# Kernel optimization log

Hardware: AMD Instinct MI355X
Metric: run time of the kernel (lower is better)

## Reference

```python
import jax, jax.numpy as jnp
import numpy as np
import math

N = 131072   # number of points
C = 32       # embed_dim
K = 19       # num_class
ZD = 16      # z_dim
BN_EPS = 1e-4
SIG_THR = 0.8


def setup_inputs():
    key = jax.random.key(0)
    ks = jax.random.split(key, 16)
    f32 = jnp.float32
    rn = lambda k, s, sc=1.0: jax.random.normal(k, s, dtype=f32) * sc
    return {
        'feat': rn(ks[0], (N, C)),
        'scene_flow': rn(ks[1], (N, 3)),
        'coarse_pred': rn(ks[2], (N, K)),
        'z': rn(ks[3], (ZD,)),
        'select_w1': rn(ks[4], (C, C), 0.2),
        'bn_gamma': jnp.ones((C,), f32),
        'bn_beta': jnp.zeros((C,), f32),
        'bn_mean': jnp.zeros((C,), f32),
        'bn_var': jnp.ones((C,), f32),
        'select_w2': rn(ks[5], (C, 1), 0.2),
        'select_b2': jnp.zeros((1,), f32),
        'wq': rn(ks[6], (C, C), 0.2), 'bq': jnp.zeros((C,), f32),
        'wk': rn(ks[7], (C, C), 0.2), 'bk': jnp.zeros((C,), f32),
        'wv': rn(ks[8], (C, C), 0.2), 'bv': jnp.zeros((C,), f32),
        'wo': rn(ks[9], (C, C), 0.2), 'bo': jnp.zeros((C,), f32),
        'wt': rn(ks[10], (2 * C, C), 0.2), 'bt': jnp.zeros((C,), f32),
        'w_out': rn(ks[11], (C, K), 0.2), 'b_out': jnp.zeros((K,), f32),
        'w_gen': rn(ks[12], (ZD + K + 3, C), 0.2), 'b_gen': jnp.zeros((C,), f32),
    }


def _forward(feat, scene_flow, coarse_pred, z, select_w1, bn_gamma, bn_beta,
             bn_mean, bn_var, select_w2, select_b2, wq, bq, wk, bk, wv, bv,
             wo, bo, wt, bt, w_out, b_out, w_gen, b_gen):
    cp = jax.nn.softmax(coarse_pred, axis=-1)                      # (N, K)
    temp_mask = jnp.any(scene_flow != 0, axis=-1)                  # (N,)
    # select_mlp: Linear(no bias) -> BatchNorm(eval, eps=1e-4) -> ReLU -> Linear -> Sigmoid
    h = (feat @ select_w1 - bn_mean) / jnp.sqrt(bn_var + BN_EPS) * bn_gamma + bn_beta
    h = jnp.maximum(h, 0.0)
    score = jax.nn.sigmoid(h @ select_w2 + select_b2)[:, 0]        # (N,)
    valid = (score < SIG_THR) & temp_mask                          # (N,)
    # cvae stand-in: linear over concat(z, onehot(class), scene_flow) -> (N, K, C)
    wz, wc, ws = w_gen[:ZD], w_gen[ZD:ZD + K], w_gen[ZD + K:]
    gen = (z @ wz + b_gen)[None, None, :] + wc[None, :, :] + (scene_flow @ ws)[:, None, :]
    gen = gen * cp[:, :, None]                                     # scale by softmax prob
    # tiny cross-attention: 1 query per point over K=19 class prototypes
    q = feat @ wq + bq                                             # (N, C)
    k_ = jnp.einsum('nkc,cd->nkd', gen, wk) + bk                   # (N, K, C)
    v_ = jnp.einsum('nkc,cd->nkd', gen, wv) + bv                   # (N, K, C)
    attn = jax.nn.softmax(jnp.einsum('nd,nkd->nk', q, k_) / math.sqrt(C), axis=-1)
    aug = jnp.einsum('nk,nkd->nd', attn, v_) @ wo + bo             # (N, C)
    # scatter-back: invalid points get zeros (equivalent to torch boolean scatter)
    new_feat = jnp.where(valid[:, None], aug, 0.0)
    refine = jnp.concatenate([feat, new_feat], axis=-1) @ wt + bt  # (N, C)
    return refine @ w_out + b_out                                  # (N, K)


def reference(feat, scene_flow, coarse_pred, z, select_w1, bn_gamma, bn_beta,
              bn_mean, bn_var, select_w2, select_b2, wq, bq, wk, bk, wv, bv,
              wo, bo, wt, bt, w_out, b_out, w_gen, b_gen):
    return _forward(feat, scene_flow, coarse_pred, z, select_w1, bn_gamma,
                    bn_beta, bn_mean, bn_var, select_w2, select_b2, wq, bq,
                    wk, bk, wv, bv, wo, bo, wt, bt, w_out, b_out, w_gen, b_gen)
```

## Files before the change

### kernel.cpp

```cpp
#include <hip/hip_runtime.h>

#define NPTS 131072

typedef __attribute__((ext_vector_type(8))) short short8;
typedef __attribute__((ext_vector_type(4))) float f32x4;

constexpr int OFF_SW1 = 0;
constexpr int OFF_BNS = 1024;
constexpr int OFF_BNH = 1056;
constexpr int OFF_SW2 = 1088;
constexpr int OFF_B2  = 1120;
constexpr int OFF_QGB = 1121;
constexpr int OFF_QMB = 1140;
constexpr int OFF_BB  = 1143;
constexpr int OFF_CV  = 1162;
constexpr int OFF_MVB = 1181;
constexpr int EGVB    = 1240;
constexpr int FRAGH   = 1620;
constexpr int FRAGL   = 2900;
constexpr int XA1 = 3412, XA2 = 4020, XG = 4628, XMK = 5236, XMV = 5332;
constexpr int XGK = 5428, XGV = 6036, XB = 6644, XQG = 7252, XQM = 7860;

#define CONST_AS __attribute__((address_space(4)))
__device__ __forceinline__ const CONST_AS float* to_const(const float* p) {
    return (const CONST_AS float*)p;
}
__device__ __forceinline__ unsigned b16r(float x) {
    unsigned u = __float_as_uint(x);
    return (u + 0x7fffu + ((u >> 16) & 1u)) >> 16;
}
__device__ __forceinline__ float fromb(unsigned h) {
    return __uint_as_float(h << 16);
}

__global__ __launch_bounds__(256) void pre_a(
    const float* __restrict__ z,
    const float* __restrict__ sw1,
    const float* __restrict__ bn_gamma, const float* __restrict__ bn_beta,
    const float* __restrict__ bn_mean,  const float* __restrict__ bn_var,
    const float* __restrict__ sw2,      const float* __restrict__ sb2,
    const float* __restrict__ wk, const float* __restrict__ wv,
    const float* __restrict__ wt, const float* __restrict__ bt,
    const float* __restrict__ wout, const float* __restrict__ bout,
    const float* __restrict__ wgen, const float* __restrict__ bgen,
    float* __restrict__ W)
{
    int i = blockIdx.x * 256 + threadIdx.x;
    if (i < 1024) {
        W[OFF_SW1 + i] = sw1[(i & 31) * 32 + (i >> 5)];
    } else if (i < 1632) {
        int t = i - 1024, e = t / 19, j = t % 19;
        float a1 = 0.f, a2 = 0.f;
        for (int d = 0; d < 32; ++d) {
            float w_ = wout[d*19 + j];
            a1 += wt[e*32 + d] * w_;
            a2 += wt[(32 + e)*32 + d] * w_;
        }
        W[XA1 + t] = a1; W[XA2 + t] = a2;
    } else if (i < 2240) {
        int t = i - 1632, k = t >> 5, e = t & 31;
        float g = bgen[e];
        for (int d = 0; d < 16; ++d) g += z[d] * wgen[d*32 + e];
        W[XG + t] = g + wgen[(16 + k)*32 + e];
    } else if (i < 2336) {
        int t = i - 2240, m = t >> 5, c = t & 31;
        float a = 0.f, b = 0.f;
        for (int e = 0; e < 32; ++e) {
            float wsr = wgen[(35 + m)*32 + e];
            a += wsr * wk[e*32 + c];
            b += wsr * wv[e*32 + c];
        }
        W[XMK + t] = a; W[XMV + t] = b;
    } else if (i < 2368) {
        int t = i - 2336;
        float scale = bn_gamma[t] / sqrtf(bn_var[t] + 1e-4f);
        W[OFF_BNS + t] = scale;
        W[OFF_BNH + t] = bn_beta[t] - bn_mean[t] * scale;
        W[OFF_SW2 + t] = sw2[t];
    } else if (i < 2387) {
        int t = i - 2368;
        float a = bout[t];
        for (int d = 0; d < 32; ++d) a += bt[d] * wout[d*19 + t];
        W[OFF_BB + t] = a;
    } else if (i == 2387) {
        W[OFF_B2] = sb2[0];
    }
}

__global__ __launch_bounds__(256) void pre_b(
    const float* __restrict__ wq, const float* __restrict__ bq,
    const float* __restrict__ wk, const float* __restrict__ wv,
    const float* __restrict__ wo,
    float* __restrict__ W)
{
    int i = blockIdx.x * 256 + threadIdx.x;
    if (i < 608) {
        int k = i >> 5, c = i & 31;
        float a = 0.f, b = 0.f;
        for (int e = 0; e < 32; ++e) {
            float g = W[XG + k*32 + e];
            a += g * wk[e*32 + c];
            b += g * wv[e*32 + c];
        }
        W[XGK + i] = a; W[XGV + i] = b;
    } else if (i < 1216) {
        int t = i - 608, c = t / 19, j = t % 19;
        float a = 0.f;
        for (int d = 0; d < 32; ++d) a += wo[c*32 + d] * W[XA2 + d*19 + j];
        W[XB + t] = a;
    } else if (i < 1312) {
        int t = i - 1216, e = t / 3, m = t % 3;
        float a = 0.f;
        for (int c = 0; c < 32; ++c) a += wq[e*32 + c] * W[XMK + m*32 + c];
        W[XQM + t] = a;
    } else if (i < 1315) {
        int m = i - 1312;
        float a = 0.f;
        for (int c = 0; c < 32; ++c) a += bq[c] * W[XMK + m*32 + c];
        W[OFF_QMB + m] = a;
    }
}

__global__ __launch_bounds__(256) void pre_c(
    const float* __restrict__ wq, const float* __restrict__ bq,
    const float* __restrict__ bv, const float* __restrict__ bo,
    float* __restrict__ W)
{
    int i = blockIdx.x * 256 + threadIdx.x;
    if (i < 608) {
        int e = i / 19, k = i % 19;
        float a = 0.f;
        for (int c = 0; c < 32; ++c) a += wq[e*32 + c] * W[XGK + k*32 + c];
        W[XQG + i] = a;
    } else if (i < 627) {
        int k = i - 608;
        float a = 0.f;
        for (int c = 0; c < 32; ++c) a += bq[c] * W[XGK + k*32 + c];
        W[OFF_QGB + k] = a;
    } else if (i < 988) {
        int t = i - 627, k = t / 19, j = t % 19;
        float a = 0.f;
        for (int c = 0; c < 32; ++c) a += W[XGV + k*32 + c] * W[XB + c*19 + j];
        W[EGVB + k*20 + j] = a;
    } else if (i < 1007) {
        int k = i - 988;
        W[EGVB + k*20 + 19] = 0.f;
    } else if (i < 1064) {
        int t = i - 1007, m = t / 19, j = t % 19;
        float a = 0.f;
        for (int c = 0; c < 32; ++c) a += W[XMV + m*32 + c] * W[XB + c*19 + j];
        W[OFF_MVB + t] = a;
    } else if (i < 1083) {
        int j = i - 1064;
        float a = 0.f;
        for (int c = 0; c < 32; ++c) a += bv[c] * W[XB + c*19 + j];
        for (int d = 0; d < 32; ++d) a += bo[d] * W[XA2 + d*19 + j];
        W[OFF_CV + j] = a;
    }
}

__global__ __launch_bounds__(256) void pre_d(
    const float* __restrict__ sw1, float* __restrict__ W)
{
    int i = blockIdx.x * 256 + threadIdx.x;
    unsigned short* FH = (unsigned short*)(W + FRAGH);
    unsigned short* FL = (unsigned short*)(W + FRAGL);
    if (i < 2560) {
        int T = i >> 9, l = (i >> 3) & 63, j = i & 7;
        int e = ((l >> 4) << 3) + j, col = 16*T + (l & 15);
        float v;
        if      (col < 32) v = sw1[e*32 + col];
        else if (col < 51) v = W[XQG + e*19 + (col - 32)];
        else if (col < 70) v = W[XA1 + e*19 + (col - 51)];
        else if (col < 73) v = W[XQM + e*3  + (col - 70)];
        else               v = 0.f;
        FH[(T*64 + l)*8 + j] = (unsigned short)b16r(v);
    } else if (i < 3584) {
        int i2 = i - 2560;
        int T = i2 >> 9, l = (i2 >> 3) & 63, j = i2 & 7;
        int e = ((l >> 4) << 3) + j, col = 16*T + (l & 15);
        float v = sw1[e*32 + col];
        float vh = fromb(b16r(v));
        FL[(T*64 + l)*8 + j] = (unsigned short)b16r(v - vh);
    }
}

__global__ __launch_bounds__(256, 2) void main_k(
    const float* __restrict__ feat,
    const float* __restrict__ sflow,
    const float* __restrict__ cpred,
    const float* __restrict__ Wg,
    float* __restrict__ out)
{
    const CONST_AS float* W = to_const(Wg);
    const int t = threadIdx.x, lane = t & 63, wvi = t >> 6;
    const int pblk = blockIdx.x * 256;

    __shared__ __align__(16) float HF[32 * 264];
    __shared__ __align__(16) unsigned short OH[41 * 264];
    __shared__ __align__(16) float GV[380];

    if (t < 95) ((float4*)GV)[t] = ((const float4*)(Wg + EGVB))[t];

    const short8* FH8 = (const short8*)(Wg + FRAGH);
    const short8* FL8 = (const short8*)(Wg + FRAGL);
    short8 bh0 = FH8[0*64 + lane], bh1 = FH8[1*64 + lane];
    short8 bh2 = FH8[2*64 + lane], bh3 = FH8[3*64 + lane];
    short8 bh4 = FH8[4*64 + lane];
    short8 bl0 = FL8[0*64 + lane], bl1 = FL8[1*64 + lane];

    const int n15 = lane & 15, q = lane >> 4;

#pragma unroll
    for (int tile = 0; tile < 4; ++tile) {
        const int p0 = wvi*64 + tile*16;
        const float* fr = feat + (long)(pblk + p0 + n15) * 32 + q*8;
        float xv[8];
        {
            float4 va = *(const float4*)fr;
            float4 vb = *(const float4*)(fr + 4);
            xv[0]=va.x; xv[1]=va.y; xv[2]=va.z; xv[3]=va.w;
            xv[4]=vb.x; xv[5]=vb.y; xv[6]=vb.z; xv[7]=vb.w;
        }
        short8 ah, al;
#pragma unroll
        for (int j = 0; j < 8; ++j) {
            unsigned h = b16r(xv[j]);
            ah[j] = (short)h;
            al[j] = (short)b16r(xv[j] - fromb(h));
        }
        f32x4 z4 = {0.f, 0.f, 0.f, 0.f};
        f32x4 aH0, aH1, a2_, a3_, a4_;
        aH0 = __builtin_amdgcn_mfma_f32_16x16x32_bf16(ah, bh0, z4, 0, 0, 0);
        aH0 = __builtin_amdgcn_mfma_f32_16x16x32_bf16(ah, bl0, aH0, 0, 0, 0);
        aH0 = __builtin_amdgcn_mfma_f32_16x16x32_bf16(al, bh0, aH0, 0, 0, 0);
        aH1 = __builtin_amdgcn_mfma_f32_16x16x32_bf16(ah, bh1, z4, 0, 0, 0);
        aH1 = __builtin_amdgcn_mfma_f32_16x16x32_bf16(ah, bl1, aH1, 0, 0, 0);
        aH1 = __builtin_amdgcn_mfma_f32_16x16x32_bf16(al, bh1, aH1, 0, 0, 0);
        a2_ = __builtin_amdgcn_mfma_f32_16x16x32_bf16(ah, bh2, z4, 0, 0, 0);
        a3_ = __builtin_amdgcn_mfma_f32_16x16x32_bf16(ah, bh3, z4, 0, 0, 0);
        a4_ = __builtin_amdgcn_mfma_f32_16x16x32_bf16(ah, bh4, z4, 0, 0, 0);

        *(f32x4*)&HF[(n15)      * 264 + p0 + q*4] = aH0;
        *(f32x4*)&HF[(16 + n15) * 264 + p0 + q*4] = aH1;
        {
            unsigned d0, d1;
            d0 = b16r(a2_[0]) | (b16r(a2_[1]) << 16);
            d1 = b16r(a2_[2]) | (b16r(a2_[3]) << 16);
            *(uint2*)&OH[(n15) * 264 + p0 + q*4] = make_uint2(d0, d1);
            d0 = b16r(a3_[0]) | (b16r(a3_[1]) << 16);
            d1 = b16r(a3_[2]) | (b16r(a3_[3]) << 16);
            *(uint2*)&OH[(16 + n15) * 264 + p0 + q*4] = make_uint2(d0, d1);
            if (n15 <= 8) {
                d0 = b16r(a4_[0]) | (b16r(a4_[1]) << 16);
                d1 = b16r(a4_[2]) | (b16r(a4_[3]) << 16);
                *(uint2*)&OH[(32 + n15) * 264 + p0 + q*4] = make_uint2(d0, d1);
            }
        }
    }
    __syncthreads();

    const long p = pblk + t;

    float s0 = sflow[p*3 + 0], s1 = sflow[p*3 + 1], s2 = sflow[p*3 + 2];
    bool tmask = (s0 != 0.f) | (s1 != 0.f) | (s2 != 0.f);

    float cp[19];
#pragma unroll
    for (int k = 0; k < 19; ++k) cp[k] = cpred[p*19 + k];
    float m1 = cp[0];
#pragma unroll
    for (int k = 1; k < 19; ++k) m1 = fmaxf(m1, cp[k]);
    float sum1 = 0.f;
#pragma unroll
    for (int k = 0; k < 19; ++k) { cp[k] = __expf(cp[k] - m1); sum1 += cp[k]; }
    float r1 = 1.f / sum1;
#pragma unroll
    for (int k = 0; k < 19; ++k) cp[k] *= r1;

    const float TH = 1.3862943611198906f;
    float sacc = W[OFF_B2];
#pragma unroll
    for (int c = 0; c < 32; ++c) {
        float a = HF[c*264 + t];
        float h = fmaxf(fmaf(a, W[OFF_BNS + c], W[OFF_BNH + c]), 0.f);
        sacc = fmaf(h, W[OFF_SW2 + c], sacc);
    }
    bool nearthr = fabsf(sacc - TH) < 1e-3f;
    if (__ballot(nearthr) != 0ULL) {
        float f[32];
        const float4* fp4 = (const float4*)(feat + p*32);
#pragma unroll
        for (int g = 0; g < 8; ++g) {
            float4 v = fp4[g];
            f[g*4+0]=v.x; f[g*4+1]=v.y; f[g*4+2]=v.z; f[g*4+3]=v.w;
        }
        float sr = W[OFF_B2];
        for (int c = 0; c < 32; ++c) {
            float a = 0.f;
#pragma unroll
            for (int e = 0; e < 32; ++e) a = fmaf(f[e], W[OFF_SW1 + c*32 + e], a);
            float h = fmaxf(fmaf(a, W[OFF_BNS + c], W[OFF_BNH + c]), 0.f);
            sr = fmaf(h, W[OFF_SW2 + c], sr);
        }
        sacc = nearthr ? sr : sacc;
    }
    bool valid = tmask && (sacc < TH);

    float qm0 = fromb(OH[38*264 + t]) + W[OFF_QMB + 0];
    float qm1 = fromb(OH[39*264 + t]) + W[OFF_QMB + 1];
    float qm2 = fromb(OH[40*264 + t]) + W[OFF_QMB + 2];
    float qs = s0*qm0 + s1*qm1 + s2*qm2;

    const float RS = 0.17677669529663687f;
    float l[19];
#pragma unroll
    for (int k = 0; k < 19; ++k)
        l[k] = (cp[k] * (fromb(OH[k*264 + t]) + W[OFF_QGB + k] + qs)) * RS;

    float m2 = l[0];
#pragma unroll
    for (int k = 1; k < 19; ++k) m2 = fmaxf(m2, l[k]);
    float sum2 = 0.f;
#pragma unroll
    for (int k = 0; k < 19; ++k) { l[k] = __expf(l[k] - m2); sum2 += l[k]; }
    float r2 = 1.f / sum2;
    float Sw = 0.f;
#pragma unroll
    for (int k = 0; k < 19; ++k) { l[k] = l[k] * r2 * cp[k]; Sw += l[k]; }

    float o[19];
#pragma unroll
    for (int j = 0; j < 19; ++j) o[j] = fromb(OH[(19 + j)*264 + t]) + W[OFF_BB + j];

    float a2[19];
    float c0 = Sw * s0, c1 = Sw * s1, c2 = Sw * s2;
#pragma unroll
    for (int j = 0; j < 19; ++j)
        a2[j] = W[OFF_CV + j] + c0 * W[OFF_MVB + j]
              + c1 * W[OFF_MVB + 19 + j] + c2 * W[OFF_MVB + 38 + j];
#pragma unroll
    for (int k = 0; k < 19; ++k) {
        float lk = l[k];
#pragma unroll
        for (int j = 0; j < 19; ++j) a2[j] = fmaf(lk, GV[k*20 + j], a2[j]);
    }

    float vg = valid ? 1.f : 0.f;
    float* op = out + p * 19;
#pragma unroll
    for (int j = 0; j < 19; ++j) op[j] = fmaf(vg, a2[j], o[j]);
}

extern "C" void kernel_launch(void* const* d_in, const int* in_sizes, int n_in,
                              void* d_out, int out_size, void* d_ws, size_t ws_size,
                              hipStream_t stream) {
    const float* feat  = (const float*)d_in[0];
    const float* sflow = (const float*)d_in[1];
    const float* cpred = (const float*)d_in[2];
    const float* z     = (const float*)d_in[3];
    const float* sw1   = (const float*)d_in[4];
    const float* bn_g  = (const float*)d_in[5];
    const float* bn_b  = (const float*)d_in[6];
    const float* bn_m  = (const float*)d_in[7];
    const float* bn_v  = (const float*)d_in[8];
    const float* sw2   = (const float*)d_in[9];
    const float* sb2   = (const float*)d_in[10];
    const float* wq    = (const float*)d_in[11];
    const float* bq    = (const float*)d_in[12];
    const float* wk    = (const float*)d_in[13];
    const float* bk    = (const float*)d_in[14];  (void)bk;
    const float* wv    = (const float*)d_in[15];
    const float* bv    = (const float*)d_in[16];
    const float* wo    = (const float*)d_in[17];
    const float* bo    = (const float*)d_in[18];
    const float* wt    = (const float*)d_in[19];
    const float* bt    = (const float*)d_in[20];
    const float* wout  = (const float*)d_in[21];
    const float* bout  = (const float*)d_in[22];
    const float* wgen  = (const float*)d_in[23];
    const float* bgen  = (const float*)d_in[24];

    float* W = (float*)d_ws;

    hipLaunchKernelGGL(pre_a, dim3(10), dim3(256), 0, stream,
                       z, sw1, bn_g, bn_b, bn_m, bn_v, sw2, sb2,
                       wk, wv, wt, bt, wout, bout, wgen, bgen, W);
    hipLaunchKernelGGL(pre_b, dim3(6), dim3(256), 0, stream,
                       wq, bq, wk, wv, wo, W);
    hipLaunchKernelGGL(pre_c, dim3(5), dim3(256), 0, stream,
                       wq, bq, bv, bo, W);
    hipLaunchKernelGGL(pre_d, dim3(14), dim3(256), 0, stream,
                       sw1, W);

    hipLaunchKernelGGL(main_k, dim3(512), dim3(256), 0, stream,
                       feat, sflow, cpred, W, (float*)d_out);
}
```

Measured before the change: 141.7 us.

## Stage coarse_pred loads and output stores through LDS; fold pre_d into earlier prep kernels

```diff
diff --git a/kernel.cpp b/kernel.cpp
--- a/kernel.cpp
+++ b/kernel.cpp
@@ -18,8 +18,8 @@
 constexpr int EGVB    = 1240;
 constexpr int FRAGH   = 1620;
 constexpr int FRAGL   = 2900;
-constexpr int XA1 = 3412, XA2 = 4020, XG = 4628, XMK = 5236, XMV = 5332;
-constexpr int XGK = 5428, XGV = 6036, XB = 6644, XQG = 7252, XQM = 7860;
+constexpr int XA2 = 4020, XG = 4628, XMK = 5236, XMV = 5332;
+constexpr int XGK = 5428, XGV = 6036, XB = 6644;
 
 #define CONST_AS __attribute__((address_space(4)))
 __device__ __forceinline__ const CONST_AS float* to_const(const float* p) {
@@ -31,6 +31,10 @@
 }
 __device__ __forceinline__ float fromb(unsigned h) {
     return __uint_as_float(h << 16);
+}
+__device__ __forceinline__ int fragidx(int e, int col) {
+    int T = col >> 4, l = (col & 15) + ((e >> 3) << 4), jj = e & 7;
+    return (T * 64 + l) * 8 + jj;
 }
 
 __global__ __launch_bounds__(256) void pre_a(
@@ -46,6 +50,8 @@
     float* __restrict__ W)
 {
     int i = blockIdx.x * 256 + threadIdx.x;
+    unsigned short* FH = (unsigned short*)(W + FRAGH);
+    unsigned short* FL = (unsigned short*)(W + FRAGL);
     if (i < 1024) {
         W[OFF_SW1 + i] = sw1[(i & 31) * 32 + (i >> 5)];
     } else if (i < 1632) {
@@ -56,7 +62,8 @@
             a1 += wt[e*32 + d] * w_;
             a2 += wt[(32 + e)*32 + d] * w_;
         }
-        W[XA1 + t] = a1; W[XA2 + t] = a2;
+        FH[fragidx(e, 51 + j)] = (unsigned short)b16r(a1);
+        W[XA2 + t] = a2;
     } else if (i < 2240) {
         int t = i - 1632, k = t >> 5, e = t & 31;
         float g = bgen[e];
@@ -84,6 +91,22 @@
         W[OFF_BB + t] = a;
     } else if (i == 2387) {
         W[OFF_B2] = sb2[0];
+    } else if (i < 3412) {
+        int idx = i - 2388;
+        int T = idx >> 9, rem = idx & 511, l = rem >> 3, j = rem & 7;
+        int e = ((l >> 4) << 3) + j, col = 16*T + (l & 15);
+        FH[(T*64 + l)*8 + j] = (unsigned short)b16r(sw1[e*32 + col]);
+    } else if (i < 4436) {
+        int idx = i - 3412;
+        int T = idx >> 9, rem = idx & 511, l = rem >> 3, j = rem & 7;
+        int e = ((l >> 4) << 3) + j, col = 16*T + (l & 15);
+        float v = sw1[e*32 + col];
+        FL[(T*64 + l)*8 + j] = (unsigned short)b16r(v - fromb(b16r(v)));
+    } else if (i < 4660) {
+        int idx = i - 4436;
+        int col = 73 + idx / 32, rem = idx & 31, q = rem >> 3, j2 = rem & 7;
+        int l = (col & 15) + (q << 4);
+        FH[(4*64 + l)*8 + j2] = 0;
     }
 }
 
@@ -94,6 +117,7 @@
     float* __restrict__ W)
 {
     int i = blockIdx.x * 256 + threadIdx.x;
+    unsigned short* FH = (unsigned short*)(W + FRAGH);
     if (i < 608) {
         int k = i >> 5, c = i & 31;
         float a = 0.f, b = 0.f;
@@ -112,7 +136,7 @@
         int t = i - 1216, e = t / 3, m = t % 3;
         float a = 0.f;
         for (int c = 0; c < 32; ++c) a += wq[e*32 + c] * W[XMK + m*32 + c];
-        W[XQM + t] = a;
+        FH[fragidx(e, 70 + m)] = (unsigned short)b16r(a);
     } else if (i < 1315) {
         int m = i - 1312;
         float a = 0.f;
@@ -127,11 +151,12 @@
     float* __restrict__ W)
 {
     int i = blockIdx.x * 256 + threadIdx.x;
+    unsigned short* FH = (unsigned short*)(W + FRAGH);
     if (i < 608) {
         int e = i / 19, k = i % 19;
         float a = 0.f;
         for (int c = 0; c < 32; ++c) a += wq[e*32 + c] * W[XGK + k*32 + c];
-        W[XQG + i] = a;
+        FH[fragidx(e, 32 + k)] = (unsigned short)b16r(a);
     } else if (i < 627) {
         int k = i - 608;
         float a = 0.f;
@@ -156,32 +181,6 @@
         for (int c = 0; c < 32; ++c) a += bv[c] * W[XB + c*19 + j];
         for (int d = 0; d < 32; ++d) a += bo[d] * W[XA2 + d*19 + j];
         W[OFF_CV + j] = a;
-    }
-}
-
-__global__ __launch_bounds__(256) void pre_d(
-    const float* __restrict__ sw1, float* __restrict__ W)
-{
-    int i = blockIdx.x * 256 + threadIdx.x;
-    unsigned short* FH = (unsigned short*)(W + FRAGH);
-    unsigned short* FL = (unsigned short*)(W + FRAGL);
-    if (i < 2560) {
-        int T = i >> 9, l = (i >> 3) & 63, j = i & 7;
-        int e = ((l >> 4) << 3) + j, col = 16*T + (l & 15);
-        float v;
-        if      (col < 32) v = sw1[e*32 + col];
-        else if (col < 51) v = W[XQG + e*19 + (col - 32)];
-        else if (col < 70) v = W[XA1 + e*19 + (col - 51)];
-        else if (col < 73) v = W[XQM + e*3  + (col - 70)];
-        else               v = 0.f;
-        FH[(T*64 + l)*8 + j] = (unsigned short)b16r(v);
-    } else if (i < 3584) {
-        int i2 = i - 2560;
-        int T = i2 >> 9, l = (i2 >> 3) & 63, j = i2 & 7;
-        int e = ((l >> 4) << 3) + j, col = 16*T + (l & 15);
-        float v = sw1[e*32 + col];
-        float vh = fromb(b16r(v));
-        FL[(T*64 + l)*8 + j] = (unsigned short)b16r(v - vh);
     }
 }
 
@@ -196,11 +195,35 @@
     const int t = threadIdx.x, lane = t & 63, wvi = t >> 6;
     const int pblk = blockIdx.x * 256;
 
-    __shared__ __align__(16) float HF[32 * 264];
+    __shared__ __align__(16) float R0[32 * 264];
     __shared__ __align__(16) unsigned short OH[41 * 264];
     __shared__ __align__(16) float GV[380];
 
     if (t < 95) ((float4*)GV)[t] = ((const float4*)(Wg + EGVB))[t];
+
+    {
+        const float4* src = (const float4*)(cpred + (long)pblk * 19);
+        float4* dst = (float4*)R0;
+        dst[t] = src[t];
+        dst[256 + t] = src[256 + t];
+        dst[512 + t] = src[512 + t];
+        dst[768 + t] = src[768 + t];
+        if (t < 192) dst[1024 + t] = src[1024 + t];
+    }
+    __syncthreads();
+    float cp[19];
+#pragma unroll
+    for (int k = 0; k < 19; ++k) cp[k] = R0[t*19 + k];
+    float m1 = cp[0];
+#pragma unroll
+    for (int k = 1; k < 19; ++k) m1 = fmaxf(m1, cp[k]);
+    float sum1 = 0.f;
+#pragma unroll
+    for (int k = 0; k < 19; ++k) { cp[k] = __expf(cp[k] - m1); sum1 += cp[k]; }
+    float r1 = 1.f / sum1;
+#pragma unroll
+    for (int k = 0; k < 19; ++k) cp[k] *= r1;
+    __syncthreads();
 
     const short8* FH8 = (const short8*)(Wg + FRAGH);
     const short8* FL8 = (const short8*)(Wg + FRAGL);
@@ -241,8 +264,8 @@
         a3_ = __builtin_amdgcn_mfma_f32_16x16x32_bf16(ah, bh3, z4, 0, 0, 0);
         a4_ = __builtin_amdgcn_mfma_f32_16x16x32_bf16(ah, bh4, z4, 0, 0, 0);
 
-        *(f32x4*)&HF[(n15)      * 264 + p0 + q*4] = aH0;
-        *(f32x4*)&HF[(16 + n15) * 264 + p0 + q*4] = aH1;
+        *(f32x4*)&R0[(n15)      * 264 + p0 + q*4] = aH0;
+        *(f32x4*)&R0[(16 + n15) * 264 + p0 + q*4] = aH1;
         {
             unsigned d0, d1;
             d0 = b16r(a2_[0]) | (b16r(a2_[1]) << 16);
@@ -265,24 +288,11 @@
     float s0 = sflow[p*3 + 0], s1 = sflow[p*3 + 1], s2 = sflow[p*3 + 2];
     bool tmask = (s0 != 0.f) | (s1 != 0.f) | (s2 != 0.f);
 
-    float cp[19];
-#pragma unroll
-    for (int k = 0; k < 19; ++k) cp[k] = cpred[p*19 + k];
-    float m1 = cp[0];
-#pragma unroll
-    for (int k = 1; k < 19; ++k) m1 = fmaxf(m1, cp[k]);
-    float sum1 = 0.f;
-#pragma unroll
-    for (int k = 0; k < 19; ++k) { cp[k] = __expf(cp[k] - m1); sum1 += cp[k]; }
-    float r1 = 1.f / sum1;
-#pragma unroll
-    for (int k = 0; k < 19; ++k) cp[k] *= r1;
-
     const float TH = 1.3862943611198906f;
     float sacc = W[OFF_B2];
 #pragma unroll
     for (int c = 0; c < 32; ++c) {
-        float a = HF[c*264 + t];
+        float a = R0[c*264 + t];
         float h = fmaxf(fmaf(a, W[OFF_BNS + c], W[OFF_BNH + c]), 0.f);
         sacc = fmaf(h, W[OFF_SW2 + c], sacc);
     }
@@ -329,27 +339,37 @@
 #pragma unroll
     for (int k = 0; k < 19; ++k) { l[k] = l[k] * r2 * cp[k]; Sw += l[k]; }
 
-    float o[19];
-#pragma unroll
-    for (int j = 0; j < 19; ++j) o[j] = fromb(OH[(19 + j)*264 + t]) + W[OFF_BB + j];
-
-    float a2[19];
+    float rv[19];
     float c0 = Sw * s0, c1 = Sw * s1, c2 = Sw * s2;
+    float vg = valid ? 1.f : 0.f;
+    float a2v[19];
 #pragma unroll
     for (int j = 0; j < 19; ++j)
-        a2[j] = W[OFF_CV + j] + c0 * W[OFF_MVB + j]
-              + c1 * W[OFF_MVB + 19 + j] + c2 * W[OFF_MVB + 38 + j];
+        a2v[j] = W[OFF_CV + j] + c0 * W[OFF_MVB + j]
+               + c1 * W[OFF_MVB + 19 + j] + c2 * W[OFF_MVB + 38 + j];
 #pragma unroll
     for (int k = 0; k < 19; ++k) {
         float lk = l[k];
 #pragma unroll
-        for (int j = 0; j < 19; ++j) a2[j] = fmaf(lk, GV[k*20 + j], a2[j]);
-    }
-
-    float vg = valid ? 1.f : 0.f;
-    float* op = out + p * 19;
-#pragma unroll
-    for (int j = 0; j < 19; ++j) op[j] = fmaf(vg, a2[j], o[j]);
+        for (int j = 0; j < 19; ++j) a2v[j] = fmaf(lk, GV[k*20 + j], a2v[j]);
+    }
+#pragma unroll
+    for (int j = 0; j < 19; ++j)
+        rv[j] = fmaf(vg, a2v[j], fromb(OH[(19 + j)*264 + t]) + W[OFF_BB + j]);
+
+    __syncthreads();
+#pragma unroll
+    for (int j = 0; j < 19; ++j) R0[t*19 + j] = rv[j];
+    __syncthreads();
+    {
+        const float4* src = (const float4*)R0;
+        float4* dst = (float4*)(out + (long)pblk * 19);
+        dst[t] = src[t];
+        dst[256 + t] = src[256 + t];
+        dst[512 + t] = src[512 + t];
+        dst[768 + t] = src[768 + t];
+        if (t < 192) dst[1024 + t] = src[1024 + t];
+    }
 }
 
 extern "C" void kernel_launch(void* const* d_in, const int* in_sizes, int n_in,
@@ -383,15 +403,13 @@
 
     float* W = (float*)d_ws;
 
-    hipLaunchKernelGGL(pre_a, dim3(10), dim3(256), 0, stream,
+    hipLaunchKernelGGL(pre_a, dim3(19), dim3(256), 0, stream,
                        z, sw1, bn_g, bn_b, bn_m, bn_v, sw2, sb2,
                        wk, wv, wt, bt, wout, bout, wgen, bgen, W);
     hipLaunchKernelGGL(pre_b, dim3(6), dim3(256), 0, stream,
                        wq, bq, wk, wv, wo, W);
     hipLaunchKernelGGL(pre_c, dim3(5), dim3(256), 0, stream,
                        wq, bq, bv, bo, W);
-    hipLaunchKernelGGL(pre_d, dim3(14), dim3(256), 0, stream,
-                       sw1, W);
 
     hipLaunchKernelGGL(main_k, dim3(512), dim3(256), 0, stream,
                        feat, sflow, cpred, W, (float*)d_out);
```

Result: no change. 140.2 us (-1.0%).
